# Performance work log

Measured on AMD Instinct MI355X. Metric: run time of the kernel, lower is better.

Reference implementation:

```python
import math
import jax, jax.numpy as jnp
import numpy as np

NUM_HEADS = 8


def _bl(x, w):
    # x: [B, ..., D], w: [B, O, D] -> [B, ..., O]
    return jnp.einsum('b...d,bod->b...o', x, w)


def setup_inputs() -> dict:
    key = jax.random.key(0)
    ks = jax.random.split(key, 5)
    B, C, P, D = 4, 16, 512, 256
    return {
        'qz': jax.random.normal(ks[0], (B, C, P, D), dtype=jnp.float32),
        'time_u': jax.random.normal(ks[1], (B, D, D), dtype=jnp.float32),
        'time_v': jax.random.normal(ks[2], (B, D, D), dtype=jnp.float32),
        'channel_u': jax.random.normal(ks[3], (B, D, D), dtype=jnp.float32),
        'channel_v': jax.random.normal(ks[4], (B, D, D), dtype=jnp.float32),
    }


def _time_msg(qz, u, v, num_heads):
    B, C, P, D = qz.shape
    H = num_heads
    R = D // H
    qu = _bl(qz, u).reshape(B, C, P, H, R).transpose(0, 1, 3, 2, 4)  # bchpr
    qv = _bl(qz, v).reshape(B, C, P, H, R).transpose(0, 1, 3, 2, 4)  # bchqr
    attn = jnp.einsum('bchpr,bchqr->bchpq', qu, qv) / math.sqrt(R)
    attn = jax.nn.softmax(attn, axis=-1)
    msg = jnp.einsum('bchpq,bcqd->bchpd', attn, qz)
    return msg.mean(axis=2)  # [B, C, P, D]


def _chan_msg(qz, u, v, num_heads):
    B, C, P, D = qz.shape
    H = num_heads
    R = D // H
    qu = _bl(qz, u).reshape(B, C, P, H, R).transpose(0, 2, 3, 1, 4)  # bphcr
    qv = _bl(qz, v).reshape(B, C, P, H, R).transpose(0, 2, 3, 1, 4)  # bphfr
    attn = jnp.einsum('bphcr,bphfr->bphcf', qu, qv) / math.sqrt(R)
    attn = jax.nn.softmax(attn, axis=-1)
    qzp = qz.transpose(0, 2, 1, 3)  # [B, P, C, D]
    msg = jnp.einsum('bphcf,bpfd->bphcd', attn, qzp).mean(axis=2)  # [B, P, C, D]
    return msg.transpose(0, 2, 1, 3)  # [B, C, P, D]


def reference(qz, time_u, time_v, channel_u, channel_v):
    m_t = _time_msg(qz, time_u, time_v, NUM_HEADS)
    m_c = _chan_msg(qz, channel_u, channel_v, NUM_HEADS)
    return (m_t, m_c)
```

## Files before the change

### kernel.cpp

```cpp
#include <hip/hip_runtime.h>
#include <hip/hip_bf16.h>
#include <stdint.h>

#define B_ 4
#define C_ 16
#define P_ 512
#define D_ 256
#define H_ 8
#define SCALE 0.17677669529663687f
#define LOG2E 1.4426950408889634f
#define NE 8388608

typedef float4 f4;
typedef uint32_t u32;
typedef __attribute__((ext_vector_type(4))) float f32x4;
typedef __attribute__((ext_vector_type(8))) short short8;

__device__ __forceinline__ unsigned short bf16bits(float x) {
  union { __hip_bfloat16 h; unsigned short u; } cv;
  cv.h = __float2bfloat16(x);
  return cv.u;
}
__device__ __forceinline__ float bf2f(unsigned short u) {
  return __uint_as_float((u32)u << 16);
}
__device__ __forceinline__ float bf2f_lo(u32 a) { return __uint_as_float(a << 16); }
__device__ __forceinline__ float bf2f_hi(u32 a) { return __uint_as_float(a & 0xffff0000u); }
__device__ __forceinline__ u32 packbf2(float a, float b) {
  return ((u32)bf16bits(b) << 16) | bf16bits(a);
}

__global__ __launch_bounds__(256)
void prep_qz(const float* __restrict__ qz, ushort* __restrict__ qzh,
             ushort* __restrict__ qzl, ushort* __restrict__ qzT) {
  const int bc = blockIdx.y;
  const int pt = blockIdx.x >> 2, dt = blockIdx.x & 3;
  const int t = threadIdx.x;
  const int row = t >> 2, cq = t & 3;
  __shared__ float T[64][65];

  const int p = pt * 64 + row;
  const int d0 = dt * 64 + cq * 16;
  const size_t base = (size_t)bc * 131072 + (size_t)p * 256 + d0;
  float v[16];
#pragma unroll
  for (int i = 0; i < 4; ++i) {
    f4 x = *(const f4*)(qz + base + i * 4);
    v[i*4+0] = x.x; v[i*4+1] = x.y; v[i*4+2] = x.z; v[i*4+3] = x.w;
  }
  ushort hs[16], ls[16];
#pragma unroll
  for (int e = 0; e < 16; ++e) {
    unsigned short hb = bf16bits(v[e]);
    hs[e] = hb;
    ls[e] = bf16bits(v[e] - bf2f(hb));
    T[cq * 16 + e][row] = v[e];
  }
  *(ushort4*)(qzh + base)     = make_ushort4(hs[0],hs[1],hs[2],hs[3]);
  *(ushort4*)(qzh + base + 4) = make_ushort4(hs[4],hs[5],hs[6],hs[7]);
  *(ushort4*)(qzh + base + 8) = make_ushort4(hs[8],hs[9],hs[10],hs[11]);
  *(ushort4*)(qzh + base +12) = make_ushort4(hs[12],hs[13],hs[14],hs[15]);
  *(ushort4*)(qzl + base)     = make_ushort4(ls[0],ls[1],ls[2],ls[3]);
  *(ushort4*)(qzl + base + 4) = make_ushort4(ls[4],ls[5],ls[6],ls[7]);
  *(ushort4*)(qzl + base + 8) = make_ushort4(ls[8],ls[9],ls[10],ls[11]);
  *(ushort4*)(qzl + base +12) = make_ushort4(ls[12],ls[13],ls[14],ls[15]);
  __syncthreads();
  const int drow = t >> 2, pq = t & 3;
  ushort os[16];
#pragma unroll
  for (int e = 0; e < 16; ++e) os[e] = bf16bits(T[drow][pq * 16 + e]);
  const size_t tbase = (size_t)bc * 131072 + (size_t)(dt * 64 + drow) * 512 + pt * 64 + pq * 16;
  *(ushort4*)(qzT + tbase)     = make_ushort4(os[0],os[1],os[2],os[3]);
  *(ushort4*)(qzT + tbase + 4) = make_ushort4(os[4],os[5],os[6],os[7]);
  *(ushort4*)(qzT + tbase + 8) = make_ushort4(os[8],os[9],os[10],os[11]);
  *(ushort4*)(qzT + tbase +12) = make_ushort4(os[12],os[13],os[14],os[15]);
}

__global__ __launch_bounds__(256)
void prep_w(const float* __restrict__ tu, const float* __restrict__ tv,
            const float* __restrict__ cu, const float* __restrict__ cv,
            ushort* __restrict__ wh, ushort* __restrict__ wl) {
  const int e4 = blockIdx.x * 256 + threadIdx.x;
  const int idx = e4 * 4;
  const int k0 = idx & 255;
  const int n  = (idx >> 8) & 511;
  const int b  = (idx >> 17) & 3;
  const int br = idx >> 19;
  const float* src;
  float sc;
  if (br == 0) {
    if (n < 256) { src = tu + ((size_t)b * 256 + n) * 256 + k0; sc = SCALE * LOG2E; }
    else         { src = tv + ((size_t)b * 256 + (n - 256)) * 256 + k0; sc = 1.f; }
  } else {
    if (n < 256) { src = cu + ((size_t)b * 256 + n) * 256 + k0; sc = SCALE * LOG2E; }
    else         { src = cv + ((size_t)b * 256 + (n - 256)) * 256 + k0; sc = 1.f; }
  }
  f4 x = *(const f4*)src;
  float v[4] = {x.x * sc, x.y * sc, x.z * sc, x.w * sc};
  ushort hs[4], ls[4];
#pragma unroll
  for (int e = 0; e < 4; ++e) {
    unsigned short hb = bf16bits(v[e]);
    hs[e] = hb;
    ls[e] = bf16bits(v[e] - bf2f(hb));
  }
  const size_t dst = ((size_t)(br * 4 + b) * 512 + n) * 256 + k0;
  *(ushort4*)(wh + dst) = make_ushort4(hs[0], hs[1], hs[2], hs[3]);
  *(ushort4*)(wl + dst) = make_ushort4(ls[0], ls[1], ls[2], ls[3]);
}

__global__ __launch_bounds__(256, 2)
void proj_all(const ushort* __restrict__ qzh, const ushort* __restrict__ qzl,
              const ushort* __restrict__ wh, const ushort* __restrict__ wl,
              ushort* __restrict__ quh, ushort* __restrict__ qul,
              ushort* __restrict__ qvh, ushort* __restrict__ qvl,
              float* __restrict__ qcu, float* __restrict__ qcv) {
  __shared__ char smem[65536];
  const int b = blockIdx.z;
  const int m0 = blockIdx.x * 128;
  const int nt = blockIdx.y;
  const int br = nt >> 2;
  const int n0l = (nt & 3) * 128;
  const int tid = threadIdx.x;
  const int w = tid >> 6, lane = tid & 63;
  const int g = lane >> 4, li = lane & 15;
  const int wm = w >> 1, wn = w & 1;

  f32x4 acc[4][4];
#pragma unroll
  for (int i = 0; i < 4; ++i)
#pragma unroll
    for (int j = 0; j < 4; ++j) acc[i][j] = f32x4{0.f,0.f,0.f,0.f};

  auto stage = [&](int buf, int ks) {
#pragma unroll
    for (int i = 0; i < 4; ++i) {
      int cch = i * 256 + tid;
      int row = cch >> 3, col = cch & 7;
      const ushort* s = (col < 4 ? qzh : qzl) + (size_t)(b * 8192 + m0 + row) * 256 + ks * 32 + (col & 3) * 8;
      uint4 v = *(const uint4*)s;
      *(uint4*)(smem + buf * 16384 + row * 128 + ((col * 16) ^ ((row & 7) << 4))) = v;
    }
#pragma unroll
    for (int i = 0; i < 4; ++i) {
      int cch = i * 256 + tid;
      int row = cch >> 3, col = cch & 7;
      const ushort* s = (col < 4 ? wh : wl) + ((size_t)(br * 4 + b) * 512 + n0l + row) * 256 + ks * 32 + (col & 3) * 8;
      uint4 v = *(const uint4*)s;
      *(uint4*)(smem + 32768 + buf * 16384 + row * 128 + ((col * 16) ^ ((row & 7) << 4))) = v;
    }
  };

  stage(0, 0);
  __syncthreads();
  int buf = 0;
  for (int ks = 0; ks < 8; ++ks) {
    if (ks < 7) stage(buf ^ 1, ks + 1);
    const char* Ab = smem + buf * 16384;
    const char* Bb = smem + 32768 + buf * 16384;
    const int sw = (li & 7) << 4;
    short8 ah[4], al[4];
#pragma unroll
    for (int mt = 0; mt < 4; ++mt) {
      int r = (wm * 64 + mt * 16 + li) * 128;
      ah[mt] = *(const short8*)(Ab + r + ((g * 16) ^ sw));
      al[mt] = *(const short8*)(Ab + r + ((64 + g * 16) ^ sw));
    }
#pragma unroll
    for (int nt2 = 0; nt2 < 4; ++nt2) {
      int r = (wn * 64 + nt2 * 16 + li) * 128;
      short8 bh = *(const short8*)(Bb + r + ((g * 16) ^ sw));
      short8 bl = *(const short8*)(Bb + r + ((64 + g * 16) ^ sw));
#pragma unroll
      for (int mt = 0; mt < 4; ++mt) {
        acc[mt][nt2] = __builtin_amdgcn_mfma_f32_16x16x32_bf16(ah[mt], bh, acc[mt][nt2], 0, 0, 0);
        acc[mt][nt2] = __builtin_amdgcn_mfma_f32_16x16x32_bf16(ah[mt], bl, acc[mt][nt2], 0, 0, 0);
        acc[mt][nt2] = __builtin_amdgcn_mfma_f32_16x16x32_bf16(al[mt], bh, acc[mt][nt2], 0, 0, 0);
      }
    }
    __syncthreads();
    buf ^= 1;
  }

#pragma unroll
  for (int mt = 0; mt < 4; ++mt) {
#pragma unroll
    for (int nt2 = 0; nt2 < 4; ++nt2) {
      int nG = n0l + wn * 64 + nt2 * 16 + li;
#pragma unroll
      for (int j = 0; j < 4; ++j) {
        int m = m0 + wm * 64 + mt * 16 + g * 4 + j;
        int cc = m >> 9, p = m & 511;
        float val = acc[mt][nt2][j];
        if (br == 0) {
          int nn = nG & 255;
          int h = nn >> 5, r = nn & 31;
          size_t dst = ((((size_t)b * 16 + cc) * 8 + h) * 512 + p) * 32 + r;
          unsigned short hb = bf16bits(val);
          unsigned short lb = bf16bits(val - bf2f(hb));
          if (nG < 256) { quh[dst] = hb; qul[dst] = lb; }
          else          { qvh[dst] = hb; qvl[dst] = lb; }
        } else {
          size_t dst = ((size_t)(b * 16 + cc) * 512 + p) * 256 + (nG & 255);
          if (nG < 256) qcu[dst] = val;
          else          qcv[dst] = val;
        }
      }
    }
  }
}

__global__ __launch_bounds__(256, 3)
void time_attn_v7(const ushort* __restrict__ quh, const ushort* __restrict__ qul,
                  const ushort* __restrict__ qvh, const ushort* __restrict__ qvl,
                  const ushort* __restrict__ qzT, float* __restrict__ out) {
  __shared__ char lds[33792];
  const int bc = blockIdx.x;
  const int q0 = blockIdx.y * 32;
  const int tid = threadIdx.x;
  const int w = tid >> 6, lane = tid & 63;
  const int g = lane >> 4, li = lane & 15;
  const int pr = w >> 1, half = w & 1;
  const int sw = (li & 7) << 4;
  float2* redml = (float2*)(lds + 32768);

  u32 macc_p[32];
#pragma unroll
  for (int i = 0; i < 32; ++i) macc_p[i] = 0u;

  int buf = 0;
#pragma unroll 1
  for (int h = 0; h < H_; ++h) {
    const size_t hb = (size_t)bc * 131072 + h * 16384;
    const size_t qoff = hb + (size_t)(q0 + pr * 16 + li) * 32 + g * 8;
    short8 bh = *(const short8*)(quh + qoff);
    short8 bl = *(const short8*)(qul + qoff);
    const ushort* kh = qvh + hb + (size_t)(half * 256 + li) * 32 + g * 8;
    const ushort* kl = qvl + hb + (size_t)(half * 256 + li) * 32 + g * 8;

    f32x4 t[16];
#pragma unroll
    for (int kt = 0; kt < 16; ++kt) {
      short8 a_h = *(const short8*)(kh + kt * 512);
      short8 a_l = *(const short8*)(kl + kt * 512);
      f32x4 a = f32x4{0.f,0.f,0.f,0.f};
      a = __builtin_amdgcn_mfma_f32_16x16x32_bf16(a_h, bh, a, 0, 0, 0);
      a = __builtin_amdgcn_mfma_f32_16x16x32_bf16(a_h, bl, a, 0, 0, 0);
      a = __builtin_amdgcn_mfma_f32_16x16x32_bf16(a_l, bh, a, 0, 0, 0);
      t[kt] = a;
      if ((kt & 3) == 3) __builtin_amdgcn_sched_barrier(0);
    }

    float m = -1e30f;
#pragma unroll
    for (int kt = 0; kt < 16; ++kt)
      m = fmaxf(m, fmaxf(fmaxf(t[kt][0], t[kt][1]), fmaxf(t[kt][2], t[kt][3])));
    m = fmaxf(m, __shfl_xor(m, 16));
    m = fmaxf(m, __shfl_xor(m, 32));

    float l = 0.f;
#pragma unroll
    for (int kt = 0; kt < 16; ++kt) {
      float e0 = exp2f(t[kt][0] - m);
      float e1 = exp2f(t[kt][1] - m);
      float e2 = exp2f(t[kt][2] - m);
      float e3 = exp2f(t[kt][3] - m);
      t[kt][0] = e0; t[kt][1] = e1; t[kt][2] = e2; t[kt][3] = e3;
      l += (e0 + e1) + (e2 + e3);
    }
    l += __shfl_xor(l, 16);
    l += __shfl_xor(l, 32);

    if (g == 0) redml[((buf * 2 + pr) * 16 + li) * 2 + half] = make_float2(m, l);
    __syncthreads();
    float2 o = redml[((buf * 2 + pr) * 16 + li) * 2 + (half ^ 1)];
    const float M = fmaxf(m, o.x);
    const float se = exp2f(m - M);
    const float lt = l * se + o.y * exp2f(o.x - M);
    const float rinv = 0.125f * se / lt;

#pragma unroll
    for (int kt = 0; kt < 16; ++kt) {
      u32 c0 = macc_p[kt*2], c1 = macc_p[kt*2+1];
      macc_p[kt*2]   = packbf2(fmaf(t[kt][0], rinv, bf2f_lo(c0)),
                               fmaf(t[kt][1], rinv, bf2f_hi(c0)));
      macc_p[kt*2+1] = packbf2(fmaf(t[kt][2], rinv, bf2f_lo(c1)),
                               fmaf(t[kt][3], rinv, bf2f_hi(c1)));
    }
    buf ^= 1;
  }

  {
    char* myrow = lds + (pr * 16 + li) * 1024;
#pragma unroll
    for (int kt = 0; kt < 16; ++kt)
      *(uint2*)(myrow + ((half * 512 + kt * 32 + g * 8) ^ sw)) =
          make_uint2(macc_p[kt*2], macc_p[kt*2+1]);
  }
  __syncthreads();

  const int rt = w & 1;
  const int d0t = (w >> 1) * 8;
  f32x4 oacc[8];
#pragma unroll
  for (int d = 0; d < 8; ++d) oacc[d] = f32x4{0.f,0.f,0.f,0.f};
  const ushort* qzTb = qzT + (size_t)bc * 131072;
#pragma unroll 2
  for (int ks = 0; ks < 16; ++ks) {
    short8 pa = *(const short8*)(lds + (rt * 16 + li) * 1024 + ((ks * 64 + g * 16) ^ sw));
#pragma unroll
    for (int d = 0; d < 8; ++d) {
      short8 bz = *(const short8*)(qzTb + (size_t)((d0t + d) * 16 + li) * 512 + ks * 32 + g * 8);
      oacc[d] = __builtin_amdgcn_mfma_f32_16x16x32_bf16(pa, bz, oacc[d], 0, 0, 0);
    }
  }
  float* outB = out + (size_t)bc * 131072;
#pragma unroll
  for (int d = 0; d < 8; ++d)
#pragma unroll
    for (int j = 0; j < 4; ++j)
      outB[(size_t)(q0 + rt * 16 + g * 4 + j) * 256 + (d0t + d) * 16 + li] = oacc[d][j];
}

__global__ __launch_bounds__(64)
void chan_attn_kernel(const float* __restrict__ qu, const float* __restrict__ qv,
                      const float* __restrict__ qz, float* __restrict__ out) {
  const int p = blockIdx.x, b = blockIdx.y;
  __shared__ float buf0[16][260];
  __shared__ float qvC[16][260];
  __shared__ float A_m[16][17];

  const int tid = threadIdx.x;
  const int f = tid & 15;
  const int gg = tid >> 4;

#pragma unroll
  for (int cc = 0; cc < 16; ++cc) {
    size_t off = (((size_t)b * C_ + cc) * P_ + p) * D_ + tid*4;
    *(f4*)&buf0[cc][tid*4] = *(const f4*)&qu[off];
    *(f4*)&qvC[cc][tid*4]  = *(const f4*)&qv[off];
  }
  __syncthreads();

  float am[4] = {0.f, 0.f, 0.f, 0.f};
  for (int h = 0; h < H_; ++h) {
    f4 vr[8];
#pragma unroll
    for (int i = 0; i < 8; ++i) vr[i] = *(const f4*)&qvC[f][h*32 + i*4];
    float sj[4];
#pragma unroll
    for (int j = 0; j < 4; ++j) {
      int cc = gg + 4*j;
      float ssum = 0.f;
#pragma unroll
      for (int i = 0; i < 8; ++i) {
        f4 uu = *(const f4*)&buf0[cc][h*32 + i*4];
        ssum += uu.x*vr[i].x + uu.y*vr[i].y + uu.z*vr[i].z + uu.w*vr[i].w;
      }
      sj[j] = ssum;
    }
#pragma unroll
    for (int j = 0; j < 4; ++j) {
      float mx = sj[j];
      for (int off = 8; off >= 1; off >>= 1) mx = fmaxf(mx, __shfl_xor(mx, off));
      float pv = exp2f(sj[j] - mx);
      float sum = pv;
      for (int off = 8; off >= 1; off >>= 1) sum += __shfl_xor(sum, off);
      am[j] += pv * (0.125f / sum);
    }
  }
#pragma unroll
  for (int j = 0; j < 4; ++j) A_m[gg + 4*j][f] = am[j];
  __syncthreads();
#pragma unroll
  for (int cc = 0; cc < 16; ++cc) {
    size_t off = (((size_t)b * C_ + cc) * P_ + p) * D_ + tid*4;
    *(f4*)&buf0[cc][tid*4] = *(const f4*)&qz[off];
  }
  __syncthreads();

  f4 acc4[16];
#pragma unroll
  for (int cc = 0; cc < 16; ++cc) acc4[cc] = make_float4(0.f, 0.f, 0.f, 0.f);
#pragma unroll
  for (int ff = 0; ff < 16; ++ff) {
    f4 z = *(const f4*)&buf0[ff][tid*4];
#pragma unroll
    for (int cc = 0; cc < 16; ++cc) {
      float aa = A_m[cc][ff];
      acc4[cc].x = fmaf(aa, z.x, acc4[cc].x);
      acc4[cc].y = fmaf(aa, z.y, acc4[cc].y);
      acc4[cc].z = fmaf(aa, z.z, acc4[cc].z);
      acc4[cc].w = fmaf(aa, z.w, acc4[cc].w);
    }
  }
#pragma unroll
  for (int cc = 0; cc < 16; ++cc) {
    size_t off = (((size_t)b * C_ + cc) * P_ + p) * D_ + tid*4;
    *(f4*)&out[off] = acc4[cc];
  }
}

extern "C" void kernel_launch(void* const* d_in, const int* in_sizes, int n_in,
                              void* d_out, int out_size, void* d_ws, size_t ws_size,
                              hipStream_t stream) {
  const float* qz = (const float*)d_in[0];
  const float* tu = (const float*)d_in[1];
  const float* tv = (const float*)d_in[2];
  const float* cu = (const float*)d_in[3];
  const float* cv = (const float*)d_in[4];
  float* out_mt = (float*)d_out;
  float* out_mc = out_mt + (size_t)NE;

  ushort* W = (ushort*)d_ws;
  ushort* qzh = W;
  ushort* qzl = qzh + NE;
  ushort* qzT = qzl + NE;
  ushort* wh  = qzT + NE;
  ushort* wl  = wh + 1048576;
  ushort* quh = wl + 1048576;
  ushort* qul = quh + NE;
  ushort* qvh = qul + NE;
  ushort* qvl = qvh + NE;
  float* qcu = out_mt;
  float* qcv = out_mc;

  hipLaunchKernelGGL(prep_qz, dim3(32, 64), dim3(256), 0, stream, qz, qzh, qzl, qzT);
  hipLaunchKernelGGL(prep_w, dim3(1024), dim3(256), 0, stream, tu, tv, cu, cv, wh, wl);
  hipLaunchKernelGGL(proj_all, dim3(64, 8, 4), dim3(256), 0, stream,
                     qzh, qzl, wh, wl, quh, qul, qvh, qvl, qcu, qcv);
  hipLaunchKernelGGL(chan_attn_kernel, dim3(P_, B_), dim3(64), 0, stream,
                     qcu, qcv, qz, out_mc);
  hipLaunchKernelGGL(time_attn_v7, dim3(64, 16), dim3(256), 0, stream,
                     quh, qul, qvh, qvl, qzT, out_mt);
}
```

Baseline: 282.7 us.

## Split time attention keys across four waves with 16-query tiles and fp32 accumulators

The time attention kernel now handles 16 queries per block instead of 32. Each of the four waves covers a quarter of the 512 keys, and the softmax statistics are merged across all four waves through LDS. The per-head probability accumulator stays in fp32 registers instead of being repacked to bf16 every head, which removes per-head pack/unpack work and improves accuracy. Smaller LDS and fewer registers permit a higher occupancy target and twice as many blocks. In exchange, the qzT operand is reloaded by twice as many blocks in the second GEMM, and each block pays more sync and reduction work per unit of output.

```diff
diff --git a/kernel.cpp b/kernel.cpp
--- a/kernel.cpp
+++ b/kernel.cpp
@@ -24,8 +24,6 @@
 __device__ __forceinline__ float bf2f(unsigned short u) {
   return __uint_as_float((u32)u << 16);
 }
-__device__ __forceinline__ float bf2f_lo(u32 a) { return __uint_as_float(a << 16); }
-__device__ __forceinline__ float bf2f_hi(u32 a) { return __uint_as_float(a & 0xffff0000u); }
 __device__ __forceinline__ u32 packbf2(float a, float b) {
   return ((u32)bf16bits(b) << 16) | bf16bits(a);
 }
@@ -210,37 +208,38 @@
   }
 }
 
-__global__ __launch_bounds__(256, 3)
-void time_attn_v7(const ushort* __restrict__ quh, const ushort* __restrict__ qul,
+__global__ __launch_bounds__(256, 5)
+void time_attn_v8(const ushort* __restrict__ quh, const ushort* __restrict__ qul,
                   const ushort* __restrict__ qvh, const ushort* __restrict__ qvl,
                   const ushort* __restrict__ qzT, float* __restrict__ out) {
-  __shared__ char lds[33792];
+  __shared__ char lds[17408];
   const int bc = blockIdx.x;
-  const int q0 = blockIdx.y * 32;
+  const int q0 = blockIdx.y * 16;
   const int tid = threadIdx.x;
   const int w = tid >> 6, lane = tid & 63;
   const int g = lane >> 4, li = lane & 15;
-  const int pr = w >> 1, half = w & 1;
   const int sw = (li & 7) << 4;
-  float2* redml = (float2*)(lds + 32768);
-
-  u32 macc_p[32];
-#pragma unroll
-  for (int i = 0; i < 32; ++i) macc_p[i] = 0u;
+  float2* redml = (float2*)(lds + 16384);
+
+  float macc[8][4];
+#pragma unroll
+  for (int kt = 0; kt < 8; ++kt)
+#pragma unroll
+    for (int j = 0; j < 4; ++j) macc[kt][j] = 0.f;
 
   int buf = 0;
 #pragma unroll 1
   for (int h = 0; h < H_; ++h) {
     const size_t hb = (size_t)bc * 131072 + h * 16384;
-    const size_t qoff = hb + (size_t)(q0 + pr * 16 + li) * 32 + g * 8;
+    const size_t qoff = hb + (size_t)(q0 + li) * 32 + g * 8;
     short8 bh = *(const short8*)(quh + qoff);
     short8 bl = *(const short8*)(qul + qoff);
-    const ushort* kh = qvh + hb + (size_t)(half * 256 + li) * 32 + g * 8;
-    const ushort* kl = qvl + hb + (size_t)(half * 256 + li) * 32 + g * 8;
-
-    f32x4 t[16];
-#pragma unroll
-    for (int kt = 0; kt < 16; ++kt) {
+    const ushort* kh = qvh + hb + (size_t)(w * 128 + li) * 32 + g * 8;
+    const ushort* kl = qvl + hb + (size_t)(w * 128 + li) * 32 + g * 8;
+
+    f32x4 t[8];
+#pragma unroll
+    for (int kt = 0; kt < 8; ++kt) {
       short8 a_h = *(const short8*)(kh + kt * 512);
       short8 a_l = *(const short8*)(kl + kt * 512);
       f32x4 a = f32x4{0.f,0.f,0.f,0.f};
@@ -253,14 +252,14 @@
 
     float m = -1e30f;
 #pragma unroll
-    for (int kt = 0; kt < 16; ++kt)
+    for (int kt = 0; kt < 8; ++kt)
       m = fmaxf(m, fmaxf(fmaxf(t[kt][0], t[kt][1]), fmaxf(t[kt][2], t[kt][3])));
     m = fmaxf(m, __shfl_xor(m, 16));
     m = fmaxf(m, __shfl_xor(m, 32));
 
     float l = 0.f;
 #pragma unroll
-    for (int kt = 0; kt < 16; ++kt) {
+    for (int kt = 0; kt < 8; ++kt) {
       float e0 = exp2f(t[kt][0] - m);
       float e1 = exp2f(t[kt][1] - m);
       float e2 = exp2f(t[kt][2] - m);
@@ -271,55 +270,53 @@
     l += __shfl_xor(l, 16);
     l += __shfl_xor(l, 32);
 
-    if (g == 0) redml[((buf * 2 + pr) * 16 + li) * 2 + half] = make_float2(m, l);
+    if (g == 0) redml[(buf * 16 + li) * 4 + w] = make_float2(m, l);
     __syncthreads();
-    float2 o = redml[((buf * 2 + pr) * 16 + li) * 2 + (half ^ 1)];
-    const float M = fmaxf(m, o.x);
-    const float se = exp2f(m - M);
-    const float lt = l * se + o.y * exp2f(o.x - M);
-    const float rinv = 0.125f * se / lt;
-
-#pragma unroll
-    for (int kt = 0; kt < 16; ++kt) {
-      u32 c0 = macc_p[kt*2], c1 = macc_p[kt*2+1];
-      macc_p[kt*2]   = packbf2(fmaf(t[kt][0], rinv, bf2f_lo(c0)),
-                               fmaf(t[kt][1], rinv, bf2f_hi(c0)));
-      macc_p[kt*2+1] = packbf2(fmaf(t[kt][2], rinv, bf2f_lo(c1)),
-                               fmaf(t[kt][3], rinv, bf2f_hi(c1)));
-    }
+    f4 r01 = ((const f4*)redml)[(buf * 16 + li) * 2 + 0];
+    f4 r23 = ((const f4*)redml)[(buf * 16 + li) * 2 + 1];
+    const float M = fmaxf(fmaxf(r01.x, r01.z), fmaxf(r23.x, r23.z));
+    const float L = r01.y * exp2f(r01.x - M) + r01.w * exp2f(r01.z - M)
+                  + r23.y * exp2f(r23.x - M) + r23.w * exp2f(r23.z - M);
+    const float rinv = 0.125f * exp2f(m - M) / L;
+
+#pragma unroll
+    for (int kt = 0; kt < 8; ++kt)
+#pragma unroll
+      for (int j = 0; j < 4; ++j)
+        macc[kt][j] = fmaf(t[kt][j], rinv, macc[kt][j]);
     buf ^= 1;
   }
 
   {
-    char* myrow = lds + (pr * 16 + li) * 1024;
-#pragma unroll
-    for (int kt = 0; kt < 16; ++kt)
-      *(uint2*)(myrow + ((half * 512 + kt * 32 + g * 8) ^ sw)) =
-          make_uint2(macc_p[kt*2], macc_p[kt*2+1]);
-  }
-  __syncthreads();
-
-  const int rt = w & 1;
-  const int d0t = (w >> 1) * 8;
-  f32x4 oacc[8];
-#pragma unroll
-  for (int d = 0; d < 8; ++d) oacc[d] = f32x4{0.f,0.f,0.f,0.f};
+    char* myrow = lds + li * 1024;
+#pragma unroll
+    for (int kt = 0; kt < 8; ++kt) {
+      u32 p0 = packbf2(macc[kt][0], macc[kt][1]);
+      u32 p1 = packbf2(macc[kt][2], macc[kt][3]);
+      *(uint2*)(myrow + ((w * 256 + kt * 32 + g * 8) ^ sw)) = make_uint2(p0, p1);
+    }
+  }
+  __syncthreads();
+
+  f32x4 oacc[4];
+#pragma unroll
+  for (int d = 0; d < 4; ++d) oacc[d] = f32x4{0.f,0.f,0.f,0.f};
   const ushort* qzTb = qzT + (size_t)bc * 131072;
 #pragma unroll 2
   for (int ks = 0; ks < 16; ++ks) {
-    short8 pa = *(const short8*)(lds + (rt * 16 + li) * 1024 + ((ks * 64 + g * 16) ^ sw));
-#pragma unroll
-    for (int d = 0; d < 8; ++d) {
-      short8 bz = *(const short8*)(qzTb + (size_t)((d0t + d) * 16 + li) * 512 + ks * 32 + g * 8);
+    short8 pa = *(const short8*)(lds + li * 1024 + ((ks * 64 + g * 16) ^ sw));
+#pragma unroll
+    for (int d = 0; d < 4; ++d) {
+      short8 bz = *(const short8*)(qzTb + (size_t)((w * 4 + d) * 16 + li) * 512 + ks * 32 + g * 8);
       oacc[d] = __builtin_amdgcn_mfma_f32_16x16x32_bf16(pa, bz, oacc[d], 0, 0, 0);
     }
   }
   float* outB = out + (size_t)bc * 131072;
 #pragma unroll
-  for (int d = 0; d < 8; ++d)
+  for (int d = 0; d < 4; ++d)
 #pragma unroll
     for (int j = 0; j < 4; ++j)
-      outB[(size_t)(q0 + rt * 16 + g * 4 + j) * 256 + (d0t + d) * 16 + li] = oacc[d][j];
+      outB[(size_t)(q0 + g * 4 + j) * 256 + w * 64 + d * 16 + li] = oacc[d][j];
 }
 
 __global__ __launch_bounds__(64)
@@ -431,6 +428,6 @@
                      qzh, qzl, wh, wl, quh, qul, qvh, qvl, qcu, qcv);
   hipLaunchKernelGGL(chan_attn_kernel, dim3(P_, B_), dim3(64), 0, stream,
                      qcu, qcv, qz, out_mc);
-  hipLaunchKernelGGL(time_attn_v7, dim3(64, 16), dim3(256), 0, stream,
+  hipLaunchKernelGGL(time_attn_v8, dim3(64, 32), dim3(256), 0, stream,
                      quh, qul, qvh, qvl, qzT, out_mt);
 }
```

After: 258.7 us. 1.09x faster.
